# Performance work log

Hardware: AMD Instinct MI355X
Metric: run time of the kernel (lower is better)

Reference implementation:

```python
import jax, jax.numpy as jnp
import numpy as np

D_MODEL = 1024
N_HEADS = 16
D_FF = 4096
EPS = 1e-5


def setup_inputs() -> dict:
    key = jax.random.key(0)
    ks = jax.random.split(key, 13)
    d, f = D_MODEL, D_FF
    s = 1.0 / np.sqrt(d)
    sf = 1.0 / np.sqrt(f)
    return {
        "x": jax.random.normal(ks[0], (2, 2048, d), dtype=jnp.float32),
        "Wq": jax.random.normal(ks[1], (d, d), dtype=jnp.float32) * s,
        "bq": jnp.zeros((d,), jnp.float32),
        "Wk": jax.random.normal(ks[2], (d, d), dtype=jnp.float32) * s,
        "bk": jnp.zeros((d,), jnp.float32),
        "Wv": jax.random.normal(ks[3], (d, d), dtype=jnp.float32) * s,
        "bv": jnp.zeros((d,), jnp.float32),
        "Wo": jax.random.normal(ks[4], (d, d), dtype=jnp.float32) * s,
        "bo": jnp.zeros((d,), jnp.float32),
        "W1": jax.random.normal(ks[5], (f, d), dtype=jnp.float32) * s,
        "b1": jnp.zeros((f,), jnp.float32),
        "W2": jax.random.normal(ks[6], (d, f), dtype=jnp.float32) * sf,
        "b2": jnp.zeros((d,), jnp.float32),
        "g1": jnp.ones((d,), jnp.float32),
        "be1": jnp.zeros((d,), jnp.float32),
        "g2": jnp.ones((d,), jnp.float32),
        "be2": jnp.zeros((d,), jnp.float32),
    }


def _layernorm(x, g, b):
    mu = jnp.mean(x, axis=-1, keepdims=True)
    var = jnp.mean(jnp.square(x - mu), axis=-1, keepdims=True)
    return (x - mu) * jax.lax.rsqrt(var + EPS) * g + b


def reference(x, Wq, bq, Wk, bk, Wv, bv, Wo, bo, W1, b1, W2, b2, g1, be1, g2, be2):
    B, S, D = x.shape
    H = N_HEADS
    dk = D // H
    # QKV projections (torch Linear: x @ W.T + b), reshape to [B,H,S,dk]
    def proj(W, b):
        return (x @ W.T + b).reshape(B, S, H, dk).transpose(0, 2, 1, 3)
    Q, K, V = proj(Wq, bq), proj(Wk, bk), proj(Wv, bv)
    scores = jnp.einsum("bhsd,bhtd->bhst", Q, K) / jnp.sqrt(jnp.float32(dk))
    attn = jax.nn.softmax(scores, axis=-1)
    ctx = jnp.einsum("bhst,bhtd->bhsd", attn, V)
    ctx = ctx.transpose(0, 2, 1, 3).reshape(B, S, D)
    attn_out = ctx @ Wo.T + bo
    x1 = _layernorm(x + attn_out, g1, be1)
    ff = jax.nn.relu(x1 @ W1.T + b1) @ W2.T + b2
    return _layernorm(x1 + ff, g2, be2)
```

## Files before the change

### kernel.cpp

```cpp
#include <hip/hip_runtime.h>

typedef unsigned short u16;
typedef unsigned int u32;
typedef unsigned long long u64;
typedef __attribute__((ext_vector_type(8))) short short8;
typedef __attribute__((ext_vector_type(4))) float f32x4;

#define D_MODEL 1024
#define SEQ 2048
#define NH 16
#define DK 64
#define DFF 4096
#define NTOK 4096
#define LOG2E 1.44269504f

__device__ __forceinline__ u16 f2bf(float f) {
    unsigned x = __builtin_bit_cast(unsigned, f);
    x = x + 0x7fffu + ((x >> 16) & 1u);
    return (u16)(x >> 16);
}

__device__ __forceinline__ float bf2f(u16 v) {
    return __builtin_bit_cast(float, (u32)v << 16);
}

__device__ __forceinline__ float fexp2(float x) {
    float r;
    asm("v_exp_f32 %0, %1" : "=v"(r) : "v"(x));
    return r;
}

__device__ __forceinline__ void gload_lds16(const void* g, void* l) {
    __builtin_amdgcn_global_load_lds(
        (__attribute__((address_space(1))) void*)g,
        (__attribute__((address_space(3))) void*)l, 16, 0, 0);
}

__device__ __forceinline__ void cvt_body(const float* __restrict__ in,
                                         u16* __restrict__ out, int blk) {
    size_t i = ((size_t)blk * 256 + threadIdx.x) * 4;
    float4 v = *(const float4*)(in + i);
    out[i + 0] = f2bf(v.x);
    out[i + 1] = f2bf(v.y);
    out[i + 2] = f2bf(v.z);
    out[i + 3] = f2bf(v.w);
}

__global__ __launch_bounds__(256) void cvt_all(
    const float* __restrict__ sx, const float* __restrict__ s0,
    const float* __restrict__ s1, const float* __restrict__ s2,
    const float* __restrict__ s3, const float* __restrict__ s4,
    const float* __restrict__ s5, u16* __restrict__ dx, u16* __restrict__ d0,
    u16* __restrict__ d1, u16* __restrict__ d2, u16* __restrict__ d3,
    u16* __restrict__ d4, u16* __restrict__ d5) {
    int f = blockIdx.x;
    if (f < 4096) {
        cvt_body(sx, dx, f);
    } else if (f < 8192) {
        int which = (f - 4096) >> 10, blk = (f - 4096) & 1023;
        const float* s = which == 0 ? s0 : which == 1 ? s1 : which == 2 ? s2 : s3;
        u16* d = which == 0 ? d0 : which == 1 ? d1 : which == 2 ? d2 : d3;
        cvt_body(s, d, blk);
    } else if (f < 12288) {
        cvt_body(s4, d4, f - 8192);
    } else {
        cvt_body(s5, d5, f - 12288);
    }
}

__device__ __forceinline__ void gemm_core64(const u16* __restrict__ A,
                                            const u16* __restrict__ W, int K,
                                            int m0, int n0, int kbase, int kl,
                                            f32x4 (&acc)[2][4]) {
    __shared__ short8 As[64][8];
    __shared__ short8 Bs[128][8];
    const int tid = threadIdx.x;
    const int lane = tid & 63, w = tid >> 6;
    const int l15 = lane & 15, lg = lane >> 4;
    const int wr = (w >> 1) * 32, wc = (w & 1) * 64;
    const int psw = l15 & 7;

#pragma unroll
    for (int i = 0; i < 2; ++i)
#pragma unroll
        for (int jj = 0; jj < 4; ++jj) acc[i][jj] = (f32x4){0.f, 0.f, 0.f, 0.f};

    for (int k0 = kbase; k0 < kbase + kl; k0 += 64) {
        __syncthreads();
#pragma unroll
        for (int jj = 0; jj < 2; ++jj) {
            int idx = jj * 256 + tid;
            int r = idx >> 3, ck = idx & 7;
            gload_lds16(A + (size_t)(m0 + r) * K + k0 + ((ck ^ (r & 7)) * 8),
                        (char*)As + (jj * 256 + w * 64) * 16);
        }
#pragma unroll
        for (int jj = 0; jj < 4; ++jj) {
            int idx = jj * 256 + tid;
            int r = idx >> 3, ck = idx & 7;
            gload_lds16(W + (size_t)(n0 + r) * K + k0 + ((ck ^ (r & 7)) * 8),
                        (char*)Bs + (jj * 256 + w * 64) * 16);
        }
        __syncthreads();

#pragma unroll
        for (int kk = 0; kk < 2; ++kk) {
            short8 af[2], bf[4];
#pragma unroll
            for (int m = 0; m < 2; ++m)
                af[m] = As[wr + m * 16 + l15][(kk * 4 + lg) ^ psw];
#pragma unroll
            for (int nn = 0; nn < 4; ++nn)
                bf[nn] = Bs[wc + nn * 16 + l15][(kk * 4 + lg) ^ psw];
#pragma unroll
            for (int m = 0; m < 2; ++m)
#pragma unroll
                for (int nn = 0; nn < 4; ++nn)
                    acc[m][nn] = __builtin_amdgcn_mfma_f32_16x16x32_bf16(
                        af[m], bf[nn], acc[m][nn], 0, 0, 0);
        }
    }
}

__global__ __launch_bounds__(256) void gemm_k64(
    const u16* __restrict__ A, const u16* __restrict__ W,
    const float* __restrict__ bias, u16* __restrict__ outb,
    u16* __restrict__ outb2, int M, int N, int K, int KZ) {
    const int f = blockIdx.x;
    const int xcd = f & 7, j = f >> 3;
    const int mi = j & 7, n = (j >> 3) & 7, kz = j >> 6;
    const int m0 = (xcd * 8 + mi) * 64, n0 = n * 128;
    const int kl = K / KZ, kbase = kz * kl;
    u16* out = kz ? outb2 : outb;

    f32x4 acc[2][4];
    gemm_core64(A, W, K, m0, n0, kbase, kl, acc);

    const int lane = threadIdx.x & 63, w = threadIdx.x >> 6;
    const int l15 = lane & 15, lg = lane >> 4;
    const int wr = (w >> 1) * 32, wc = (w & 1) * 64;
#pragma unroll
    for (int m = 0; m < 2; ++m)
#pragma unroll
        for (int nn = 0; nn < 4; ++nn) {
            int gn = n0 + wc + nn * 16 + l15;
            float bv = (kz == 0) ? bias[gn] : 0.f;
#pragma unroll
            for (int r = 0; r < 4; ++r) {
                int gm = m0 + wr + m * 16 + lg * 4 + r;
                out[(size_t)gm * N + gn] = f2bf(acc[m][nn][r] + bv);
            }
        }
}

__global__ __launch_bounds__(256) void gemm_k64_relu(
    const u16* __restrict__ A, const u16* __restrict__ W,
    const float* __restrict__ bias, u16* __restrict__ outb, int M, int N,
    int K) {
    const int f = blockIdx.x;
    const int xcd = f & 7, j = f >> 3;
    const int mi = j & 7, n = j >> 3;
    const int m0 = (xcd * 8 + mi) * 64, n0 = n * 128;

    f32x4 acc[2][4];
    gemm_core64(A, W, K, m0, n0, 0, K, acc);

    const int lane = threadIdx.x & 63, w = threadIdx.x >> 6;
    const int l15 = lane & 15, lg = lane >> 4;
    const int wr = (w >> 1) * 32, wc = (w & 1) * 64;
#pragma unroll
    for (int m = 0; m < 2; ++m)
#pragma unroll
        for (int nn = 0; nn < 4; ++nn) {
            int gn = n0 + wc + nn * 16 + l15;
            float bv = bias[gn];
#pragma unroll
            for (int r = 0; r < 4; ++r) {
                int gm = m0 + wr + m * 16 + lg * 4 + r;
                outb[(size_t)gm * N + gn] = f2bf(fmaxf(acc[m][nn][r] + bv, 0.f));
            }
        }
}

__global__ __launch_bounds__(256) void gemm_qkv(
    const u16* __restrict__ A, const u16* __restrict__ Wq,
    const u16* __restrict__ Wk, const u16* __restrict__ Wv,
    const float* __restrict__ bq, const float* __restrict__ bk,
    const float* __restrict__ bv, u16* __restrict__ Qo, u16* __restrict__ Ko,
    u16* __restrict__ Vo) {
    const int f = blockIdx.x;
    const int xcd = f & 7, j = f >> 3;
    const int mi = j & 7, q = j >> 3;
    const int mat = q >> 3;
    const int m0 = (xcd * 8 + mi) * 64, n0 = (q & 7) * 128;
    const u16* W = mat == 0 ? Wq : (mat == 1 ? Wk : Wv);
    const float* bias = mat == 0 ? bq : (mat == 1 ? bk : bv);
    const float scale = (mat == 0) ? 0.125f * LOG2E : 1.0f;

    f32x4 acc[2][4];
    gemm_core64(A, W, D_MODEL, m0, n0, 0, D_MODEL, acc);

    const int lane = threadIdx.x & 63, w = threadIdx.x >> 6;
    const int l15 = lane & 15, lg = lane >> 4;
    const int wr = (w >> 1) * 32, wc = (w & 1) * 64;

    if (mat == 2) {
#pragma unroll
        for (int m = 0; m < 2; ++m)
#pragma unroll
            for (int nn = 0; nn < 4; ++nn) {
                int gn = n0 + wc + nn * 16 + l15;
                float bv2 = bias[gn];
                int h = gn >> 6, d = gn & 63;
                int gm0 = m0 + wr + m * 16 + lg * 4;
                int b = gm0 >> 11, s = gm0 & 2047;
                u64 pk = (u64)f2bf(acc[m][nn][0] + bv2) |
                         ((u64)f2bf(acc[m][nn][1] + bv2) << 16) |
                         ((u64)f2bf(acc[m][nn][2] + bv2) << 32) |
                         ((u64)f2bf(acc[m][nn][3] + bv2) << 48);
                size_t obase = (size_t)(b * NH + h) * DK * SEQ;
                int soff = (s & ~63) + ((((s >> 3) & 7) ^ (d & 7)) << 3) + (s & 7);
                *(u64*)(Vo + obase + (size_t)d * SEQ + soff) = pk;
            }
    } else {
        u16* out = mat == 0 ? Qo : Ko;
#pragma unroll
        for (int m = 0; m < 2; ++m)
#pragma unroll
            for (int nn = 0; nn < 4; ++nn) {
                int gn = n0 + wc + nn * 16 + l15;
                float bv2 = bias[gn];
                int h = gn >> 6, d = gn & 63;
#pragma unroll
                for (int r = 0; r < 4; ++r) {
                    int gm = m0 + wr + m * 16 + lg * 4 + r;
                    int b = gm >> 11, s = gm & 2047;
                    float v = (acc[m][nn][r] + bv2) * scale;
                    out[(((size_t)(b * NH + h)) * SEQ + s) * DK + d] = f2bf(v);
                }
            }
    }
}

__global__ __launch_bounds__(512) void attn_fwd(const u16* __restrict__ Q,
                                                const u16* __restrict__ Kp,
                                                const u16* __restrict__ Vg_,
                                                u16* __restrict__ ctx) {
    __shared__ __align__(16) u16 Kt[2][128 * 64];
    __shared__ __align__(16) u16 Vt[2][64 * 128];
    __shared__ __align__(16) u16 Ps[8][16 * 64];

    const int tid = threadIdx.x;
    const int lane = tid & 63;
    const int w = tid >> 6;
    const int l15 = lane & 15;
    const int lg = lane >> 4;
    const int f = blockIdx.x + 16 * blockIdx.y;
    const int bh = f & 31;
    const int qblk = f >> 5;
    const int qbase = qblk * 128 + w * 16;
    const u16* Qb = Q + (size_t)bh * SEQ * DK;
    const u16* Kb = Kp + (size_t)bh * SEQ * DK;
    const u16* Vg = Vg_ + (size_t)bh * DK * SEQ;

    short8 qf[2];
#pragma unroll
    for (int hf = 0; hf < 2; ++hf)
        qf[hf] = *(const short8*)(Qb + (size_t)(qbase + l15) * DK + hf * 32 + lg * 8);

    short8 onesf;
#pragma unroll
    for (int e = 0; e < 8; ++e) onesf[e] = (short)0x3F80;

    f32x4 zero = {0.f, 0.f, 0.f, 0.f};
    f32x4 o[4], o1 = zero;
#pragma unroll
    for (int db = 0; db < 4; ++db) o[db] = zero;
    float m_own = 0.f;

    u16* Pu = Ps[w];
    const int psw = l15 & 7;

#define STAGE_V(T0, BUF)                                                       \
    {                                                                          \
        _Pragma("unroll") for (int j = 0; j < 2; ++j) {                        \
            int idx = j * 512 + tid;                                           \
            gload_lds16(Vg + (size_t)(idx >> 4) * SEQ + (T0) + (idx & 15) * 8, \
                        (char*)Vt[BUF] + (j * 512 + w * 64) * 16);             \
        }                                                                      \
    }
#define STAGE_K(T0, BUF)                                                       \
    {                                                                          \
        _Pragma("unroll") for (int j = 0; j < 2; ++j) {                        \
            int idx = j * 512 + tid;                                           \
            int kv = idx >> 3, ck = idx & 7;                                   \
            gload_lds16(Kb + (size_t)((T0) + kv) * DK + ((ck ^ (kv & 7)) * 8), \
                        (char*)Kt[BUF] + (j * 512 + w * 64) * 16);             \
        }                                                                      \
    }
#define KF(BUF, H, NB, HALF)                                                   \
    (*(const short8*)((const char*)Kt[BUF] + ((H)*64 + (NB)*16 + l15) * 128 +  \
                      (((((HALF)*4 + lg)) ^ psw) << 4)))

#define ATTN_TILE(BUF, H)                                                      \
    {                                                                          \
        f32x4 seed = {-m_own, -m_own, -m_own, -m_own};                         \
        f32x4 sc[4];                                                           \
        __builtin_amdgcn_s_setprio(1);                                         \
        _Pragma("unroll") for (int nb = 0; nb < 4; ++nb) {                     \
            sc[nb] = __builtin_amdgcn_mfma_f32_16x16x32_bf16(                  \
                KF(BUF, H, nb, 0), qf[0], seed, 0, 0, 0);                      \
            sc[nb] = __builtin_amdgcn_mfma_f32_16x16x32_bf16(                  \
                KF(BUF, H, nb, 1), qf[1], sc[nb], 0, 0, 0);                    \
        }                                                                      \
        __builtin_amdgcn_s_setprio(0);                                         \
        float a0 = fmaxf(fmaxf(sc[0][0], sc[0][1]), sc[0][2]);                 \
        float a1 = fmaxf(fmaxf(sc[0][3], sc[1][0]), sc[1][1]);                 \
        float a2 = fmaxf(fmaxf(sc[1][2], sc[1][3]), sc[2][0]);                 \
        float a3 = fmaxf(fmaxf(sc[2][1], sc[2][2]), sc[2][3]);                 \
        float a4 = fmaxf(fmaxf(sc[3][0], sc[3][1]), sc[3][2]);                 \
        float lm = fmaxf(fmaxf(fmaxf(a0, a1), a2),                             \
                         fmaxf(fmaxf(a3, a4), sc[3][3]));                      \
        if (__any(lm > 8.f)) {                                                 \
            float rv = fmaxf(lm, __shfl_xor(lm, 16));                          \
            rv = fmaxf(rv, __shfl_xor(rv, 32));                                \
            float rvp = fmaxf(rv, 0.f);                                        \
            float fac = fexp2(-rvp);                                           \
            m_own += rvp;                                                      \
            _Pragma("unroll") for (int nb = 0; nb < 4; ++nb)                   \
                _Pragma("unroll") for (int r = 0; r < 4; ++r)                  \
                    sc[nb][r] -= rvp;                                          \
            _Pragma("unroll") for (int r = 0; r < 4; ++r) {                    \
                float fr = __shfl(fac, lg * 4 + r);                            \
                o1[r] *= fr;                                                   \
                _Pragma("unroll") for (int db = 0; db < 4; ++db)               \
                    o[db][r] *= fr;                                            \
            }                                                                  \
        }                                                                      \
        _Pragma("unroll") for (int nb = 0; nb < 4; ++nb) {                     \
            float p0 = fexp2(sc[nb][0]);                                       \
            float p1 = fexp2(sc[nb][1]);                                       \
            float p2 = fexp2(sc[nb][2]);                                       \
            float p3 = fexp2(sc[nb][3]);                                       \
            u32 pk01 = __builtin_amdgcn_perm(__builtin_bit_cast(u32, p1),      \
                                             __builtin_bit_cast(u32, p0),      \
                                             0x07060302u);                     \
            u32 pk23 = __builtin_amdgcn_perm(__builtin_bit_cast(u32, p3),      \
                                             __builtin_bit_cast(u32, p2),      \
                                             0x07060302u);                     \
            int ck = (nb * 2 + (lg >> 1)) ^ psw;                               \
            u64* dst = (u64*)(Pu + l15 * 64 + ck * 8 + (lg & 1) * 4);          \
            *dst = (u64)pk01 | ((u64)pk23 << 32);                              \
        }                                                                      \
        short8 pa[2];                                                          \
        _Pragma("unroll") for (int ts = 0; ts < 2; ++ts)                       \
            pa[ts] = *(const short8*)(Pu + l15 * 64 + (((ts * 4 + lg) ^ psw) * 8)); \
        __builtin_amdgcn_s_setprio(1);                                         \
        _Pragma("unroll") for (int db = 0; db < 4; ++db) {                     \
            const int d = db * 16 + l15;                                       \
            _Pragma("unroll") for (int ts = 0; ts < 2; ++ts) {                 \
                short8 vb = *(const short8*)((const char*)Vt[BUF] + d * 256 +  \
                                             (((H)*8 + (((ts * 4 + lg) ^ psw))) << 4)); \
                o[db] = __builtin_amdgcn_mfma_f32_16x16x32_bf16(               \
                    pa[ts], vb, o[db], 0, 0, 0);                               \
            }                                                                  \
        }                                                                      \
        o1 = __builtin_amdgcn_mfma_f32_16x16x32_bf16(pa[0], onesf, o1, 0, 0, 0); \
        o1 = __builtin_amdgcn_mfma_f32_16x16x32_bf16(pa[1], onesf, o1, 0, 0, 0); \
        __builtin_amdgcn_s_setprio(0);                                         \
    }

    STAGE_K(0, 0);
    STAGE_V(0, 0);

    for (int t0 = 0; t0 < SEQ; t0 += 256) {
        __syncthreads();
        STAGE_K(t0 + 128, 1);
        STAGE_V(t0 + 128, 1);
        ATTN_TILE(0, 0);
        ATTN_TILE(0, 1);
        __syncthreads();
        if (t0 + 256 < SEQ) {
            STAGE_K(t0 + 256, 0);
            STAGE_V(t0 + 256, 0);
        }
        ATTN_TILE(1, 0);
        ATTN_TILE(1, 1);
    }

    const int b = bh >> 4, h = bh & 15;
#pragma unroll
    for (int r = 0; r < 4; ++r) {
        float inv = 1.0f / o1[r];
        int srow = qbase + lg * 4 + r;
        size_t rowoff = ((size_t)(b * SEQ + srow)) * D_MODEL + h * DK;
#pragma unroll
        for (int db = 0; db < 4; ++db)
            ctx[rowoff + db * 16 + l15] = f2bf(o[db][r] * inv);
    }
#undef STAGE_V
#undef STAGE_K
#undef KF
#undef ATTN_TILE
}

template <bool XBF>
__global__ __launch_bounds__(256) void ln_res(const void* __restrict__ Xv,
                                              const u16* __restrict__ Y,
                                              const u16* __restrict__ Y2,
                                              const float* __restrict__ gamma,
                                              const float* __restrict__ beta,
                                              float* __restrict__ outf,
                                              u16* __restrict__ outb) {
    __shared__ float red[8];
    const int row = blockIdx.x, t = threadIdx.x;
    const size_t off = (size_t)row * D_MODEL + t * 4;
    float x0, x1_, x2, x3;
    if (XBF) {
        ushort4 xv = *(const ushort4*)((const u16*)Xv + off);
        x0 = bf2f(xv.x); x1_ = bf2f(xv.y); x2 = bf2f(xv.z); x3 = bf2f(xv.w);
    } else {
        float4 xv = *(const float4*)((const float*)Xv + off);
        x0 = xv.x; x1_ = xv.y; x2 = xv.z; x3 = xv.w;
    }
    ushort4 yv = *(const ushort4*)(Y + off);
    float sx = x0 + bf2f(yv.x), sy = x1_ + bf2f(yv.y);
    float sz = x2 + bf2f(yv.z), sw = x3 + bf2f(yv.w);
    if (Y2) {
        ushort4 y2 = *(const ushort4*)(Y2 + off);
        sx += bf2f(y2.x); sy += bf2f(y2.y); sz += bf2f(y2.z); sw += bf2f(y2.w);
    }
    float ps = sx + sy + sz + sw;
#pragma unroll
    for (int o2 = 32; o2; o2 >>= 1) ps += __shfl_xor(ps, o2);
    if ((t & 63) == 0) red[t >> 6] = ps;
    __syncthreads();
    float mu = (red[0] + red[1] + red[2] + red[3]) * (1.0f / D_MODEL);
    float d0 = sx - mu, d1 = sy - mu, d2 = sz - mu, d3 = sw - mu;
    float p2 = d0 * d0 + d1 * d1 + d2 * d2 + d3 * d3;
#pragma unroll
    for (int o2 = 32; o2; o2 >>= 1) p2 += __shfl_xor(p2, o2);
    if ((t & 63) == 0) red[4 + (t >> 6)] = p2;
    __syncthreads();
    float var = (red[4] + red[5] + red[6] + red[7]) * (1.0f / D_MODEL);
    float rstd = rsqrtf(var + 1e-5f);
    float4 gv = *(const float4*)(gamma + t * 4);
    float4 bv = *(const float4*)(beta + t * 4);
    float r0 = d0 * rstd * gv.x + bv.x;
    float r1 = d1 * rstd * gv.y + bv.y;
    float r2 = d2 * rstd * gv.z + bv.z;
    float r3 = d3 * rstd * gv.w + bv.w;
    if (outf) {
        float4 res; res.x = r0; res.y = r1; res.z = r2; res.w = r3;
        *(float4*)(outf + off) = res;
    }
    if (outb) {
        outb[off + 0] = f2bf(r0);
        outb[off + 1] = f2bf(r1);
        outb[off + 2] = f2bf(r2);
        outb[off + 3] = f2bf(r3);
    }
}

extern "C" void kernel_launch(void* const* d_in, const int* in_sizes, int n_in,
                              void* d_out, int out_size, void* d_ws, size_t ws_size,
                              hipStream_t stream) {
    (void)in_sizes; (void)n_in; (void)out_size; (void)ws_size;
    const float* x  = (const float*)d_in[0];
    const float* Wq = (const float*)d_in[1];
    const float* bq = (const float*)d_in[2];
    const float* Wk = (const float*)d_in[3];
    const float* bk = (const float*)d_in[4];
    const float* Wv = (const float*)d_in[5];
    const float* bv = (const float*)d_in[6];
    const float* Wo = (const float*)d_in[7];
    const float* bo = (const float*)d_in[8];
    const float* W1 = (const float*)d_in[9];
    const float* b1 = (const float*)d_in[10];
    const float* W2 = (const float*)d_in[11];
    const float* b2 = (const float*)d_in[12];
    const float* g1 = (const float*)d_in[13];
    const float* be1 = (const float*)d_in[14];
    const float* g2 = (const float*)d_in[15];
    const float* be2 = (const float*)d_in[16];

    char* ws = (char*)d_ws;
    u16* xb   = (u16*)(ws);
    u16* Qb   = (u16*)(ws + ((size_t)8 << 20));
    u16* Kb   = (u16*)(ws + ((size_t)16 << 20));
    u16* x1b  = (u16*)(ws + ((size_t)24 << 20));
    u16* W1b  = (u16*)(ws + ((size_t)32 << 20));
    u16* W2b  = (u16*)(ws + ((size_t)40 << 20));
    u16* Fs   = (u16*)(ws + ((size_t)48 << 20));
    u16* Fs2  = (u16*)(ws + ((size_t)56 << 20));
    u16* hb   = (u16*)(ws + ((size_t)64 << 20));
    u16* Wqb = hb;
    u16* Wkb = hb + (1u << 20);
    u16* Wvb = hb + (2u << 20);
    u16* Wob = hb + (3u << 20);
    u16* Vtg = Fs;
    u16* ctxb = xb;

    cvt_all<<<dim3(16384), 256, 0, stream>>>(x, Wq, Wk, Wv, Wo, W1, W2,
                                             xb, Wqb, Wkb, Wvb, Wob, W1b, W2b);

    gemm_qkv<<<dim3(1536), 256, 0, stream>>>(xb, Wqb, Wkb, Wvb, bq, bk, bv,
                                             Qb, Kb, Vtg);

    attn_fwd<<<dim3(SEQ / 128, 32), 512, 0, stream>>>(Qb, Kb, Vtg, ctxb);

    gemm_k64<<<dim3(512), 256, 0, stream>>>(ctxb, Wob, bo, Fs, nullptr,
                                            NTOK, D_MODEL, D_MODEL, 1);

    ln_res<false><<<dim3(NTOK), 256, 0, stream>>>(x, Fs, nullptr, g1, be1,
                                                  nullptr, x1b);

    gemm_k64_relu<<<dim3(2048), 256, 0, stream>>>(x1b, W1b, b1, hb,
                                                  NTOK, DFF, D_MODEL);

    gemm_k64<<<dim3(1024), 256, 0, stream>>>(hb, W2b, b2, Fs, Fs2,
                                             NTOK, D_MODEL, DFF, 2);

    ln_res<true><<<dim3(NTOK), 256, 0, stream>>>(x1b, Fs, Fs2, g2, be2,
                                                 (float*)d_out, nullptr);
}
```

Measured before the change: 227.8 us.

## Shrink attention KV tile to 64 with padded P stride; split-K Wo GEMM

The attention kernel now stages 64-key K/V tiles per buffer instead of 128, halving shared memory and doing one tile per sync phase. The per-wave P scratch gets a padded row stride of 72 to cut LDS bank conflicts. This lowers LDS usage, which may allow more blocks per CU, at the cost of twice as many barriers per sequence. Separately, the output-projection GEMM is split two ways along K into two partial buffers that the following layernorm sums, doubling its grid.

```diff
diff --git a/kernel.cpp b/kernel.cpp
--- a/kernel.cpp
+++ b/kernel.cpp
@@ -242,13 +242,15 @@
     }
 }
 
+#define KVB 64
+#define PSTR 72
 __global__ __launch_bounds__(512) void attn_fwd(const u16* __restrict__ Q,
                                                 const u16* __restrict__ Kp,
                                                 const u16* __restrict__ Vg_,
                                                 u16* __restrict__ ctx) {
-    __shared__ __align__(16) u16 Kt[2][128 * 64];
-    __shared__ __align__(16) u16 Vt[2][64 * 128];
-    __shared__ __align__(16) u16 Ps[8][16 * 64];
+    __shared__ __align__(16) u16 Kt[2][64 * 64];
+    __shared__ __align__(16) u16 Vt[2][64 * 64];
+    __shared__ __align__(16) u16 Ps[8][16 * PSTR];
 
     const int tid = threadIdx.x;
     const int lane = tid & 63;
@@ -283,35 +285,29 @@
 
 #define STAGE_V(T0, BUF)                                                       \
     {                                                                          \
-        _Pragma("unroll") for (int j = 0; j < 2; ++j) {                        \
-            int idx = j * 512 + tid;                                           \
-            gload_lds16(Vg + (size_t)(idx >> 4) * SEQ + (T0) + (idx & 15) * 8, \
-                        (char*)Vt[BUF] + (j * 512 + w * 64) * 16);             \
-        }                                                                      \
+        gload_lds16(Vg + (size_t)(tid >> 3) * SEQ + (T0) + (tid & 7) * 8,      \
+                    (char*)Vt[BUF] + (w * 64) * 16);                           \
     }
 #define STAGE_K(T0, BUF)                                                       \
     {                                                                          \
-        _Pragma("unroll") for (int j = 0; j < 2; ++j) {                        \
-            int idx = j * 512 + tid;                                           \
-            int kv = idx >> 3, ck = idx & 7;                                   \
-            gload_lds16(Kb + (size_t)((T0) + kv) * DK + ((ck ^ (kv & 7)) * 8), \
-                        (char*)Kt[BUF] + (j * 512 + w * 64) * 16);             \
-        }                                                                      \
-    }
-#define KF(BUF, H, NB, HALF)                                                   \
-    (*(const short8*)((const char*)Kt[BUF] + ((H)*64 + (NB)*16 + l15) * 128 +  \
+        int kv = tid >> 3, ck = tid & 7;                                       \
+        gload_lds16(Kb + (size_t)((T0) + kv) * DK + ((ck ^ (kv & 7)) * 8),     \
+                    (char*)Kt[BUF] + (w * 64) * 16);                           \
+    }
+#define KF(BUF, NB, HALF)                                                      \
+    (*(const short8*)((const char*)Kt[BUF] + ((NB)*16 + l15) * 128 +           \
                       (((((HALF)*4 + lg)) ^ psw) << 4)))
 
-#define ATTN_TILE(BUF, H)                                                      \
+#define ATTN_TILE(BUF)                                                         \
     {                                                                          \
         f32x4 seed = {-m_own, -m_own, -m_own, -m_own};                         \
         f32x4 sc[4];                                                           \
         __builtin_amdgcn_s_setprio(1);                                         \
         _Pragma("unroll") for (int nb = 0; nb < 4; ++nb) {                     \
             sc[nb] = __builtin_amdgcn_mfma_f32_16x16x32_bf16(                  \
-                KF(BUF, H, nb, 0), qf[0], seed, 0, 0, 0);                      \
+                KF(BUF, nb, 0), qf[0], seed, 0, 0, 0);                         \
             sc[nb] = __builtin_amdgcn_mfma_f32_16x16x32_bf16(                  \
-                KF(BUF, H, nb, 1), qf[1], sc[nb], 0, 0, 0);                    \
+                KF(BUF, nb, 1), qf[1], sc[nb], 0, 0, 0);                       \
         }                                                                      \
         __builtin_amdgcn_s_setprio(0);                                         \
         float a0 = fmaxf(fmaxf(sc[0][0], sc[0][1]), sc[0][2]);                 \
@@ -349,18 +345,19 @@
                                              __builtin_bit_cast(u32, p2),      \
                                              0x07060302u);                     \
             int ck = (nb * 2 + (lg >> 1)) ^ psw;                               \
-            u64* dst = (u64*)(Pu + l15 * 64 + ck * 8 + (lg & 1) * 4);          \
+            u64* dst = (u64*)(Pu + l15 * PSTR + ck * 8 + (lg & 1) * 4);        \
             *dst = (u64)pk01 | ((u64)pk23 << 32);                              \
         }                                                                      \
         short8 pa[2];                                                          \
         _Pragma("unroll") for (int ts = 0; ts < 2; ++ts)                       \
-            pa[ts] = *(const short8*)(Pu + l15 * 64 + (((ts * 4 + lg) ^ psw) * 8)); \
+            pa[ts] = *(const short8*)(Pu + l15 * PSTR +                        \
+                                      (((ts * 4 + lg) ^ psw) * 8));            \
         __builtin_amdgcn_s_setprio(1);                                         \
         _Pragma("unroll") for (int db = 0; db < 4; ++db) {                     \
             const int d = db * 16 + l15;                                       \
             _Pragma("unroll") for (int ts = 0; ts < 2; ++ts) {                 \
-                short8 vb = *(const short8*)((const char*)Vt[BUF] + d * 256 +  \
-                                             (((H)*8 + (((ts * 4 + lg) ^ psw))) << 4)); \
+                short8 vb = *(const short8*)((const char*)Vt[BUF] + d * 128 +  \
+                                             (((ts * 4 + lg) ^ psw) << 4));    \
                 o[db] = __builtin_amdgcn_mfma_f32_16x16x32_bf16(               \
                     pa[ts], vb, o[db], 0, 0, 0);                               \
             }                                                                  \
@@ -373,19 +370,17 @@
     STAGE_K(0, 0);
     STAGE_V(0, 0);
 
-    for (int t0 = 0; t0 < SEQ; t0 += 256) {
+    for (int t0 = 0; t0 < SEQ; t0 += 2 * KVB) {
         __syncthreads();
-        STAGE_K(t0 + 128, 1);
-        STAGE_V(t0 + 128, 1);
-        ATTN_TILE(0, 0);
-        ATTN_TILE(0, 1);
+        STAGE_K(t0 + KVB, 1);
+        STAGE_V(t0 + KVB, 1);
+        ATTN_TILE(0);
         __syncthreads();
-        if (t0 + 256 < SEQ) {
-            STAGE_K(t0 + 256, 0);
-            STAGE_V(t0 + 256, 0);
+        if (t0 + 2 * KVB < SEQ) {
+            STAGE_K(t0 + 2 * KVB, 0);
+            STAGE_V(t0 + 2 * KVB, 0);
         }
-        ATTN_TILE(1, 0);
-        ATTN_TILE(1, 1);
+        ATTN_TILE(1);
     }
 
     const int b = bh >> 4, h = bh & 15;
@@ -509,10 +504,10 @@
 
     attn_fwd<<<dim3(SEQ / 128, 32), 512, 0, stream>>>(Qb, Kb, Vtg, ctxb);
 
-    gemm_k64<<<dim3(512), 256, 0, stream>>>(ctxb, Wob, bo, Fs, nullptr,
-                                            NTOK, D_MODEL, D_MODEL, 1);
-
-    ln_res<false><<<dim3(NTOK), 256, 0, stream>>>(x, Fs, nullptr, g1, be1,
+    gemm_k64<<<dim3(1024), 256, 0, stream>>>(ctxb, Wob, bo, Fs, Fs2,
+                                             NTOK, D_MODEL, D_MODEL, 2);
+
+    ln_res<false><<<dim3(NTOK), 256, 0, stream>>>(x, Fs, Fs2, g1, be1,
                                                   nullptr, x1b);
 
     gemm_k64_relu<<<dim3(2048), 256, 0, stream>>>(x1b, W1b, b1, hb,
```

Measured after the change: 246.9 us. +8.4%, slower.
